# Kernel optimization log

Hardware: AMD Instinct MI355X
Metric: run time of the kernel (lower is better)

## Reference

```python
import jax, jax.numpy as jnp
import numpy as np

DIM = 16
HEADS = 2
EPS = 1e-5


def _layer_norm(x, g, b):
    m = x.mean(-1, keepdims=True)
    v = ((x - m) ** 2).mean(-1, keepdims=True)
    return (x - m) * jax.lax.rsqrt(v + EPS) * g + b


def setup_inputs() -> dict:
    key = jax.random.key(0)
    ks = jax.random.split(key, 8)
    B, Lq, Lk, D = 4, 2048, 2048, DIM
    xavier = float(np.sqrt(6.0 / (D + D)))  # xavier_uniform bound for square Linear
    inp = {
        "query": jax.random.normal(ks[0], (B, Lq, D), jnp.float32),
        "key": jax.random.normal(ks[1], (B, Lk, D), jnp.float32),
        "value": jax.random.normal(ks[2], (B, Lk, D), jnp.float32),
        "w": jax.random.normal(ks[3], (B, HEADS, Lq, Lk), jnp.float32) * 0.1,
        "mask": jnp.zeros((B, HEADS, Lq, Lk), jnp.float32),
        # LayerNorm params (q, k, v)
        "ln_qg": jnp.ones((D,), jnp.float32), "ln_qb": jnp.zeros((D,), jnp.float32),
        "ln_kg": jnp.ones((D,), jnp.float32), "ln_kb": jnp.zeros((D,), jnp.float32),
        "ln_vg": jnp.ones((D,), jnp.float32), "ln_vb": jnp.zeros((D,), jnp.float32),
        # Linear projections, torch layout [out, in]
        "Wq": jax.random.uniform(ks[4], (D, D), jnp.float32, -xavier, xavier),
        "bq": jnp.zeros((D,), jnp.float32),
        "Wk": jax.random.uniform(ks[5], (D, D), jnp.float32, -xavier, xavier),
        "bk": jnp.zeros((D,), jnp.float32),
        "Wv": jax.random.uniform(ks[6], (D, D), jnp.float32, -xavier, xavier),
        "bv": jnp.zeros((D,), jnp.float32),
        "Wo": jax.random.normal(ks[7], (D, D), jnp.float32) * (1.0 / np.sqrt(D)),
        "bo": jnp.zeros((D,), jnp.float32),
    }
    return inp


def reference(query, key, value, w, mask,
              ln_qg, ln_qb, ln_kg, ln_kb, ln_vg, ln_vb,
              Wq, bq, Wk, bk, Wv, bv, Wo, bo):
    B, Lq, D = query.shape
    H = HEADS
    dh = D // H
    q = _layer_norm(query, ln_qg, ln_qb)
    k = _layer_norm(key, ln_kg, ln_kb)
    v = _layer_norm(value, ln_vg, ln_vb)
    q0 = q  # residual is post-LayerNorm query
    # torch Linear: x @ W.T + b ; split heads -> [B, H, L, dh]
    Q = (q @ Wq.T + bq).reshape(B, Lq, H, dh).transpose(0, 2, 1, 3)
    K = (k @ Wk.T + bk).reshape(B, -1, H, dh).transpose(0, 2, 1, 3)
    V = (v @ Wv.T + bv).reshape(B, -1, H, dh).transpose(0, 2, 1, 3)
    Q = Q / (dh ** 0.5)
    scores = jnp.einsum('bhqd,bhkd->bhqk', Q, K) + w
    scores = scores - scores.max(axis=-1, keepdims=True)
    scores = scores + mask
    attn = jax.nn.softmax(scores, axis=-1)  # dropout is identity in eval
    ctx = jnp.einsum('bhqk,bhkd->bhqd', attn, V)
    ctx = ctx.transpose(0, 2, 1, 3).reshape(B, Lq, D)
    out = ctx @ Wo.T + bo + q0
    return out, attn
```

## Files before the change

### kernel.cpp

```cpp
#include <hip/hip_runtime.h>
#include <math.h>

#define BATCH 4
#define LQ 2048
#define LK 2048
#define DIM 16
#define HEADS 2
#define DH 8
#define EPS 1e-5f

typedef float fvec4 __attribute__((ext_vector_type(4)));
typedef unsigned int uvec4 __attribute__((ext_vector_type(4)));
typedef unsigned int uvec2 __attribute__((ext_vector_type(2)));
typedef __fp16 hvec2 __attribute__((ext_vector_type(2)));

__device__ __forceinline__ hvec2 u2h(unsigned u) {
    union { unsigned u; hvec2 h; } c; c.u = u; return c.h;
}
__device__ __forceinline__ unsigned h2u(hvec2 h) {
    union { unsigned u; hvec2 h; } c; c.h = h; return c.u;
}

__global__ __launch_bounds__(256) void ln_proj3_kernel(
    const float* __restrict__ xq, const float* __restrict__ xk,
    const float* __restrict__ xv,
    const float* __restrict__ gq, const float* __restrict__ bq_ln,
    const float* __restrict__ gk, const float* __restrict__ bk_ln,
    const float* __restrict__ gv, const float* __restrict__ bv_ln,
    const float* __restrict__ Wq, const float* __restrict__ bq,
    const float* __restrict__ Wk, const float* __restrict__ bk,
    const float* __restrict__ Wv, const float* __restrict__ bv,
    float* __restrict__ Qb, unsigned* __restrict__ Kh,
    unsigned short* __restrict__ Vh, float* __restrict__ q0)
{
    const int gid = blockIdx.x * blockDim.x + threadIdx.x;
    const int which = gid >> 13;
    const int r     = gid & 8191;

    const float* x; const float* g; const float* bl;
    const float* W; const float* bb; float scale;
    if (which == 0)      { x = xq; g = gq; bl = bq_ln; W = Wq; bb = bq; scale = 0.35355339059327373f; }
    else if (which == 1) { x = xk; g = gk; bl = bk_ln; W = Wk; bb = bk; scale = 1.0f; }
    else                 { x = xv; g = gv; bl = bv_ln; W = Wv; bb = bv; scale = 1.0f; }

    float xv16[16];
    const float4* xp = (const float4*)(x + (size_t)r * 16);
#pragma unroll
    for (int i = 0; i < 4; ++i) {
        float4 t = xp[i];
        xv16[4*i+0] = t.x; xv16[4*i+1] = t.y; xv16[4*i+2] = t.z; xv16[4*i+3] = t.w;
    }
    float m = 0.f;
#pragma unroll
    for (int i = 0; i < 16; ++i) m += xv16[i];
    m *= (1.f / 16.f);
    float var = 0.f;
#pragma unroll
    for (int i = 0; i < 16; ++i) { float d = xv16[i] - m; var += d * d; }
    var *= (1.f / 16.f);
    float rs = rsqrtf(var + EPS);

    float xn[16];
#pragma unroll
    for (int i = 0; i < 16; ++i) xn[i] = (xv16[i] - m) * rs * g[i] + bl[i];

    if (which == 0) {
        float4* op = (float4*)(q0 + (size_t)r * 16);
#pragma unroll
        for (int i = 0; i < 4; ++i) {
            float4 t; t.x = xn[4*i+0]; t.y = xn[4*i+1]; t.z = xn[4*i+2]; t.w = xn[4*i+3];
            op[i] = t;
        }
    }

    float pr[16];
#pragma unroll
    for (int j = 0; j < 16; ++j) {
        float acc = bb[j];
#pragma unroll
        for (int i = 0; i < 16; ++i) acc += xn[i] * W[j * 16 + i];
        pr[j] = acc * scale;
    }

    const int b = r >> 11;
    const int l = r & 2047;
    if (which == 0) {
#pragma unroll
        for (int j = 0; j < 16; ++j) {
            int h = j >> 3, d = j & 7;
            Qb[((((size_t)b * HEADS + h) * 2048) + l) * DH + d] = pr[j];
        }
    } else if (which == 1) {
#pragma unroll
        for (int h = 0; h < 2; ++h) {
            unsigned* Kpan = Kh + ((size_t)(b * 2 + h)) * 8192;
#pragma unroll
            for (int p = 0; p < 4; ++p) {
                hvec2 hk = __builtin_amdgcn_cvt_pkrtz(pr[h * 8 + 2 * p], pr[h * 8 + 2 * p + 1]);
                Kpan[p * 2048 + l] = h2u(hk);
            }
        }
    } else {
#pragma unroll
        for (int h = 0; h < 2; ++h) {
            unsigned short* Vpan = Vh + ((size_t)(b * 2 + h)) * 16384;
#pragma unroll
            for (int d = 0; d < 8; ++d) {
                union { __fp16 h; unsigned short u; } cv;
                cv.h = (__fp16)pr[h * 8 + d];
                Vpan[d * 2048 + l] = cv.u;
            }
        }
    }
}

__device__ __forceinline__ float wave_sum(float v) {
#pragma unroll
    for (int off = 32; off > 0; off >>= 1) v += __shfl_xor(v, off);
    return v;
}

__global__ __launch_bounds__(512, 2) void attn_kernel(
    const float* __restrict__ Q,
    const unsigned* __restrict__ Kh,
    const unsigned* __restrict__ Vh,
    const float* __restrict__ w,
    const float* __restrict__ mask,
    float* __restrict__ attn_out,
    float* __restrict__ ctx)
{
    __shared__ unsigned Kp[4][1024];
    __shared__ unsigned Vp[8][512];

    const int t    = threadIdx.x;
    const int lane = t & 63;
    const int wid  = t >> 6;
    const int bh   = blockIdx.x >> 8;
    const int qbase= (blockIdx.x & 255) << 3;
    const int q    = qbase + wid;
    const int rowid= (bh << 11) + q;
    const int h    = bh & (HEADS - 1);
    const int b    = bh >> 1;

    const unsigned* Kpan = Kh + (size_t)bh * 8192;
    const unsigned* Vpan = Vh + (size_t)bh * 8192;

    const float* Qrow = Q + (size_t)rowid * DH;
    hvec2 qpk[4];
#pragma unroll
    for (int p = 0; p < 4; ++p) qpk[p] = __builtin_amdgcn_cvt_pkrtz(Qrow[2 * p], Qrow[2 * p + 1]);

    const float* wrow = w    + (size_t)rowid * LK;
    const float* mrow = mask + (size_t)rowid * LK;

    unsigned epk[16];
    float sum = 0.f;
    float cd[8] = {0,0,0,0,0,0,0,0};

#pragma unroll
    for (int chunk = 0; chunk < 2; ++chunk) {
        if (chunk) __syncthreads();
        {
            const int gcol = (chunk << 10) + (t << 1);
#pragma unroll
            for (int p = 0; p < 4; ++p)
                *(uvec2*)&Kp[p][t << 1] = *(const uvec2*)&Kpan[p * 2048 + gcol];
#pragma unroll
            for (int d = 0; d < 8; ++d)
                Vp[d][t] = Vpan[d * 1024 + (chunk << 9) + t];
        }
        __syncthreads();
#pragma unroll
        for (int i = 0; i < 4; ++i) {
            const int cb  = (i << 8) + (lane << 2);
            const int col = (chunk << 10) + cb;
            fvec4 wv = __builtin_nontemporal_load((const fvec4*)(wrow + col));
            fvec4 mv = __builtin_nontemporal_load((const fvec4*)(mrow + col));
            uvec4 kk0 = *(const uvec4*)&Kp[0][cb];
            uvec4 kk1 = *(const uvec4*)&Kp[1][cb];
            uvec4 kk2 = *(const uvec4*)&Kp[2][cb];
            uvec4 kk3 = *(const uvec4*)&Kp[3][cb];
            float e[4];
#pragma unroll
            for (int j = 0; j < 4; ++j) {
                float sj = wv[j] + mv[j] - 4.0f;
                sj = __builtin_amdgcn_fdot2(qpk[0], u2h(kk0[j]), sj, false);
                sj = __builtin_amdgcn_fdot2(qpk[1], u2h(kk1[j]), sj, false);
                sj = __builtin_amdgcn_fdot2(qpk[2], u2h(kk2[j]), sj, false);
                sj = __builtin_amdgcn_fdot2(qpk[3], u2h(kk3[j]), sj, false);
                e[j] = __expf(sj);
            }
            sum += (e[0] + e[1]) + (e[2] + e[3]);
            hvec2 e01 = __builtin_amdgcn_cvt_pkrtz(e[0], e[1]);
            hvec2 e23 = __builtin_amdgcn_cvt_pkrtz(e[2], e[3]);
            const int g = (chunk << 2) + i;
            epk[2 * g]     = h2u(e01);
            epk[2 * g + 1] = h2u(e23);
            const int cp = cb >> 1;
#pragma unroll
            for (int d = 0; d < 8; ++d) {
                uvec2 vv = *(const uvec2*)&Vp[d][cp];
                cd[d] = __builtin_amdgcn_fdot2(e01, u2h(vv.x), cd[d], false);
                cd[d] = __builtin_amdgcn_fdot2(e23, u2h(vv.y), cd[d], false);
            }
        }
    }

    sum = wave_sum(sum);
    const float inv = 1.f / sum;

    float* arow = attn_out + (size_t)rowid * LK;
#pragma unroll
    for (int g = 0; g < 8; ++g) {
        const int col = ((g >> 2) << 10) + ((g & 3) << 8) + (lane << 2);
        hvec2 e01 = u2h(epk[2 * g]), e23 = u2h(epk[2 * g + 1]);
        fvec4 o;
        o.x = (float)e01.x * inv; o.y = (float)e01.y * inv;
        o.z = (float)e23.x * inv; o.w = (float)e23.y * inv;
        __builtin_nontemporal_store(o, (fvec4*)(arow + col));
    }

#pragma unroll
    for (int d = 0; d < 8; ++d) cd[d] = wave_sum(cd[d]) * inv;
    if (lane == 0) {
        float* cp = ctx + ((((size_t)b * LQ + q) * HEADS) + h) * DH;
        fvec4 t0; t0.x = cd[0]; t0.y = cd[1]; t0.z = cd[2]; t0.w = cd[3];
        fvec4 t1; t1.x = cd[4]; t1.y = cd[5]; t1.z = cd[6]; t1.w = cd[7];
        ((fvec4*)cp)[0] = t0;
        ((fvec4*)cp)[1] = t1;
    }
}

__global__ __launch_bounds__(256) void out_kernel(
    const float* __restrict__ ctx,
    const float* __restrict__ Wo,
    const float* __restrict__ bo,
    const float* __restrict__ q0,
    float* __restrict__ out, int n)
{
    int gid = blockIdx.x * blockDim.x + threadIdx.x;
    if (gid >= n) return;
    int row = gid >> 4, j = gid & 15;
    const float* c = ctx + (size_t)row * 16;
    float acc = bo[j];
#pragma unroll
    for (int i = 0; i < 16; ++i) acc += c[i] * Wo[j * 16 + i];
    out[gid] = acc + q0[gid];
}

extern "C" void kernel_launch(void* const* d_in, const int* in_sizes, int n_in,
                              void* d_out, int out_size, void* d_ws, size_t ws_size,
                              hipStream_t stream) {
    const float* query = (const float*)d_in[0];
    const float* key_  = (const float*)d_in[1];
    const float* value = (const float*)d_in[2];
    const float* w     = (const float*)d_in[3];
    const float* mask  = (const float*)d_in[4];
    const float* ln_qg = (const float*)d_in[5];
    const float* ln_qb = (const float*)d_in[6];
    const float* ln_kg = (const float*)d_in[7];
    const float* ln_kb = (const float*)d_in[8];
    const float* ln_vg = (const float*)d_in[9];
    const float* ln_vb = (const float*)d_in[10];
    const float* Wq = (const float*)d_in[11];
    const float* bq = (const float*)d_in[12];
    const float* Wk = (const float*)d_in[13];
    const float* bk = (const float*)d_in[14];
    const float* Wv = (const float*)d_in[15];
    const float* bv = (const float*)d_in[16];
    const float* Wo = (const float*)d_in[17];
    const float* bo = (const float*)d_in[18];

    float* out  = (float*)d_out;
    float* attn = out + (size_t)BATCH * LQ * DIM;

    const size_t NE = (size_t)BATCH * LQ * DIM;
    float* ws  = (float*)d_ws;
    float* Qb  = ws;
    float* q0  = Qb + NE;
    float* ctx = q0 + NE;
    unsigned* Kh = (unsigned*)(ctx + NE);
    unsigned short* Vh16 = (unsigned short*)(Kh + 65536);
    unsigned* Vh = (unsigned*)Vh16;

    ln_proj3_kernel<<<(3 * 8192) / 256, 256, 0, stream>>>(
        query, key_, value,
        ln_qg, ln_qb, ln_kg, ln_kb, ln_vg, ln_vb,
        Wq, bq, Wk, bk, Wv, bv,
        Qb, Kh, Vh16, q0);

    attn_kernel<<<BATCH * HEADS * LQ / 8, 512, 0, stream>>>(
        Qb, Kh, Vh, w, mask, attn, ctx);

    out_kernel<<<((int)NE + 255) / 256, 256, 0, stream>>>(
        ctx, Wo, bo, q0, out, (int)NE);
}
```

Before: 85.13 us.

## Stage full K/V panel in LDS once and prefetch w/mask rows ahead

The kernel now loads the whole K and V half-precision panels for the head into shared memory in one pass, which removes the second chunk and its extra barrier. It also issues the first four w/mask vector loads before the barrier and software-pipelines the rest, so each iteration prefetches the loads four groups ahead. LDS per block doubles to 64 KB, which may limit the two-blocks-per-CU occupancy target, and holding the prefetch buffers raises register pressure.

```diff
diff --git a/kernel.cpp b/kernel.cpp
--- a/kernel.cpp
+++ b/kernel.cpp
@@ -129,8 +129,8 @@
     float* __restrict__ attn_out,
     float* __restrict__ ctx)
 {
-    __shared__ unsigned Kp[4][1024];
-    __shared__ unsigned Vp[8][512];
+    __shared__ unsigned Kp[4][2048];
+    __shared__ unsigned Vp[8][1024];
 
     const int t    = threadIdx.x;
     const int lane = t & 63;
@@ -145,6 +145,24 @@
     const unsigned* Kpan = Kh + (size_t)bh * 8192;
     const unsigned* Vpan = Vh + (size_t)bh * 8192;
 
+    {
+        const int c = t << 1;
+#pragma unroll
+        for (int half = 0; half < 2; ++half) {
+            const int cc = c + (half << 10);
+#pragma unroll
+            for (int p = 0; p < 4; ++p)
+                *(uvec2*)&Kp[p][cc] = *(const uvec2*)&Kpan[p * 2048 + cc];
+        }
+#pragma unroll
+        for (int half = 0; half < 2; ++half) {
+            const int cp = t + (half << 9);
+#pragma unroll
+            for (int d = 0; d < 8; ++d)
+                Vp[d][cp] = Vpan[d * 1024 + cp];
+        }
+    }
+
     const float* Qrow = Q + (size_t)rowid * DH;
     hvec2 qpk[4];
 #pragma unroll
@@ -152,57 +170,55 @@
 
     const float* wrow = w    + (size_t)rowid * LK;
     const float* mrow = mask + (size_t)rowid * LK;
+
+    fvec4 wb[4], mb[4];
+#pragma unroll
+    for (int g = 0; g < 4; ++g) {
+        const int col = (g << 8) + (lane << 2);
+        wb[g] = __builtin_nontemporal_load((const fvec4*)(wrow + col));
+        mb[g] = __builtin_nontemporal_load((const fvec4*)(mrow + col));
+    }
+
+    __syncthreads();
 
     unsigned epk[16];
     float sum = 0.f;
     float cd[8] = {0,0,0,0,0,0,0,0};
 
 #pragma unroll
-    for (int chunk = 0; chunk < 2; ++chunk) {
-        if (chunk) __syncthreads();
-        {
-            const int gcol = (chunk << 10) + (t << 1);
-#pragma unroll
-            for (int p = 0; p < 4; ++p)
-                *(uvec2*)&Kp[p][t << 1] = *(const uvec2*)&Kpan[p * 2048 + gcol];
-#pragma unroll
-            for (int d = 0; d < 8; ++d)
-                Vp[d][t] = Vpan[d * 1024 + (chunk << 9) + t];
-        }
-        __syncthreads();
-#pragma unroll
-        for (int i = 0; i < 4; ++i) {
-            const int cb  = (i << 8) + (lane << 2);
-            const int col = (chunk << 10) + cb;
-            fvec4 wv = __builtin_nontemporal_load((const fvec4*)(wrow + col));
-            fvec4 mv = __builtin_nontemporal_load((const fvec4*)(mrow + col));
-            uvec4 kk0 = *(const uvec4*)&Kp[0][cb];
-            uvec4 kk1 = *(const uvec4*)&Kp[1][cb];
-            uvec4 kk2 = *(const uvec4*)&Kp[2][cb];
-            uvec4 kk3 = *(const uvec4*)&Kp[3][cb];
-            float e[4];
-#pragma unroll
-            for (int j = 0; j < 4; ++j) {
-                float sj = wv[j] + mv[j] - 4.0f;
-                sj = __builtin_amdgcn_fdot2(qpk[0], u2h(kk0[j]), sj, false);
-                sj = __builtin_amdgcn_fdot2(qpk[1], u2h(kk1[j]), sj, false);
-                sj = __builtin_amdgcn_fdot2(qpk[2], u2h(kk2[j]), sj, false);
-                sj = __builtin_amdgcn_fdot2(qpk[3], u2h(kk3[j]), sj, false);
-                e[j] = __expf(sj);
-            }
-            sum += (e[0] + e[1]) + (e[2] + e[3]);
-            hvec2 e01 = __builtin_amdgcn_cvt_pkrtz(e[0], e[1]);
-            hvec2 e23 = __builtin_amdgcn_cvt_pkrtz(e[2], e[3]);
-            const int g = (chunk << 2) + i;
-            epk[2 * g]     = h2u(e01);
-            epk[2 * g + 1] = h2u(e23);
-            const int cp = cb >> 1;
-#pragma unroll
-            for (int d = 0; d < 8; ++d) {
-                uvec2 vv = *(const uvec2*)&Vp[d][cp];
-                cd[d] = __builtin_amdgcn_fdot2(e01, u2h(vv.x), cd[d], false);
-                cd[d] = __builtin_amdgcn_fdot2(e23, u2h(vv.y), cd[d], false);
-            }
+    for (int i = 0; i < 8; ++i) {
+        fvec4 wv = wb[i & 3], mv = mb[i & 3];
+        if (i < 4) {
+            const int ncol = ((i + 4) << 8) + (lane << 2);
+            wb[i & 3] = __builtin_nontemporal_load((const fvec4*)(wrow + ncol));
+            mb[i & 3] = __builtin_nontemporal_load((const fvec4*)(mrow + ncol));
+        }
+        const int cb = (i << 8) + (lane << 2);
+        uvec4 kk0 = *(const uvec4*)&Kp[0][cb];
+        uvec4 kk1 = *(const uvec4*)&Kp[1][cb];
+        uvec4 kk2 = *(const uvec4*)&Kp[2][cb];
+        uvec4 kk3 = *(const uvec4*)&Kp[3][cb];
+        float e[4];
+#pragma unroll
+        for (int j = 0; j < 4; ++j) {
+            float sj = wv[j] + mv[j] - 4.0f;
+            sj = __builtin_amdgcn_fdot2(qpk[0], u2h(kk0[j]), sj, false);
+            sj = __builtin_amdgcn_fdot2(qpk[1], u2h(kk1[j]), sj, false);
+            sj = __builtin_amdgcn_fdot2(qpk[2], u2h(kk2[j]), sj, false);
+            sj = __builtin_amdgcn_fdot2(qpk[3], u2h(kk3[j]), sj, false);
+            e[j] = __expf(sj);
+        }
+        sum += (e[0] + e[1]) + (e[2] + e[3]);
+        hvec2 e01 = __builtin_amdgcn_cvt_pkrtz(e[0], e[1]);
+        hvec2 e23 = __builtin_amdgcn_cvt_pkrtz(e[2], e[3]);
+        epk[2 * i]     = h2u(e01);
+        epk[2 * i + 1] = h2u(e23);
+        const int cp = cb >> 1;
+#pragma unroll
+        for (int d = 0; d < 8; ++d) {
+            uvec2 vv = *(const uvec2*)&Vp[d][cp];
+            cd[d] = __builtin_amdgcn_fdot2(e01, u2h(vv.x), cd[d], false);
+            cd[d] = __builtin_amdgcn_fdot2(e23, u2h(vv.y), cd[d], false);
         }
     }
 
@@ -212,7 +228,7 @@
     float* arow = attn_out + (size_t)rowid * LK;
 #pragma unroll
     for (int g = 0; g < 8; ++g) {
-        const int col = ((g >> 2) << 10) + ((g & 3) << 8) + (lane << 2);
+        const int col = (g << 8) + (lane << 2);
         hvec2 e01 = u2h(epk[2 * g]), e23 = u2h(epk[2 * g + 1]);
         fvec4 o;
         o.x = (float)e01.x * inv; o.y = (float)e01.y * inv;
```

Measured after the change: 83.98 us. No clear change (-1.4%).
